# Kernel tuning notes

Hardware: AMD Instinct MI355X
Metric: run time of the kernel (lower is better)

## Reference

```python
import jax, jax.numpy as jnp
import numpy as np

VOCAB, D_MODEL, D_STATE, D_LATENT = 32000, 1024, 16, 32
SEQ, MAX_ITERS, TOL = 8192, 20, 1e-5


def _linear_params(k, out_d, in_d):
    lim = 1.0 / np.sqrt(in_d)  # eqx.nn.Linear default uniform init
    kw, kb = jax.random.split(k)
    W = jax.random.uniform(kw, (out_d, in_d), minval=-lim, maxval=lim, dtype=jnp.float32)
    b = jax.random.uniform(kb, (out_d,), minval=-lim, maxval=lim, dtype=jnp.float32)
    return W, b


def setup_inputs() -> dict:
    key = jax.random.key(0)
    ks = jax.random.split(key, 8)
    tokens = jax.random.randint(ks[0], (SEQ,), 0, VOCAB)
    emb = jax.random.normal(ks[1], (VOCAB, D_MODEL), dtype=jnp.float32) * 0.02
    Wf, bf = _linear_params(ks[2], D_LATENT // 2, D_STATE + D_MODEL)
    Wf2, bf2 = _linear_params(ks[3], D_LATENT // 2, D_STATE + D_MODEL)
    Wlam, blam = _linear_params(ks[4], D_STATE, D_LATENT + D_MODEL)
    Wu, bu = _linear_params(ks[5], D_STATE, D_LATENT + D_MODEL)
    Wout, bout = _linear_params(ks[6], D_MODEL, D_LATENT + D_STATE)
    return {"tokens": tokens, "emb": emb, "Wf": Wf, "bf": bf, "Wf2": Wf2, "bf2": bf2,
            "Wlam": Wlam, "blam": blam, "Wu": Wu, "bu": bu, "Wout": Wout, "bout": bout}


def reference(tokens, emb, Wf, bf, Wf2, bf2, Wlam, blam, Wu, bu, Wout, bout):
    x = emb[tokens]  # [S, d_model]

    def compute_lambda_u(z):
        zx = jnp.concatenate([z, x], axis=-1)              # [S, d_latent+d_model]
        lam = jax.nn.sigmoid(zx @ Wlam.T + blam)           # [S, d_state]
        u = zx @ Wu.T + bu                                 # [S, d_state]
        return lam, u

    def scan_h(lam, u):
        # h_t = lam_t * h_{t-1} + u_t via associative scan
        def binop(left, right):
            a1, b1 = left
            a2, b2 = right
            return (a1 * a2, a2 * b1 + b2)
        _, h = jax.lax.associative_scan(binop, (lam, u), axis=0)
        return h

    def f_theta(z, h_prev):
        hx = jnp.concatenate([h_prev, x], axis=-1)         # [S, d_state+d_model]
        alpha = jax.nn.sigmoid(hx @ Wf.T + bf)             # [S, d_latent//2]
        sigma = jax.nn.sigmoid(hx @ Wf2.T + bf2)
        u, v = jnp.split(z, 2, axis=-1)
        rho, beta, gamma = 30.0, 15.6, 0.26
        thresh = jnp.tanh(rho * (v - u))
        du = 1.0 - alpha * jnp.exp(beta * v) * (1.0 - gamma * (0.3 - u)) + sigma * thresh
        dv = -1.0 + alpha * jnp.exp(beta * u) * (1.0 + gamma * (0.3 - v)) + sigma * thresh
        return z + 0.001 * jnp.concatenate([du, dv], axis=-1)

    # Bounded fixed-point iteration with convergence freeze (emulates while_loop)
    def body(carry, _):
        z, z_prev, done = carry
        done = done | (jnp.linalg.norm(z - z_prev) < TOL)
        lam, u = compute_lambda_u(z)
        h = scan_h(lam, u)
        h_prev = jnp.concatenate([jnp.zeros((1, D_STATE), z.dtype), h[:-1]], axis=0)
        z_new = f_theta(z, h_prev)
        z_out = jnp.where(done, z, z_new)
        zp_out = jnp.where(done, z_prev, z)
        return (z_out, zp_out, done), None

    z0 = jnp.zeros((SEQ, D_LATENT), jnp.float32)
    zp0 = jnp.full((SEQ, D_LATENT), jnp.inf, jnp.float32)
    (z_star, _, _), _ = jax.lax.scan(body, (z0, zp0, jnp.array(False)), None, length=MAX_ITERS)

    lam, u = compute_lambda_u(z_star)
    h_star = scan_h(lam, u)
    zh = jnp.concatenate([z_star, h_star], axis=-1)        # [S, d_latent+d_state]
    return zh @ Wout.T + bout                              # [S, d_model]
```

## Files before the change

kernel.cpp:

```cpp
#include <hip/hip_runtime.h>

#define SEQ     8192
#define DM      1024
#define NB      256
#define CH      32
#define HALO    32
#define W       64
#define NT      512
#define MAXITERS 20

__device__ __forceinline__ float sigmoidf(float x) {
    return 1.0f / (1.0f + __expf(-x));
}
__device__ __forceinline__ float tanh_fast(float x) {
    const float e = __expf(2.0f * x);
    return 1.0f - 2.0f / (e + 1.0f);
}

__global__ __launch_bounds__(256) void k1_embed_proj(
    const int* __restrict__ tokens, const float* __restrict__ emb,
    const float* __restrict__ Wf,  const float* __restrict__ bf,
    const float* __restrict__ Wf2, const float* __restrict__ bf2,
    const float* __restrict__ Wlam,const float* __restrict__ blam,
    const float* __restrict__ Wu,  const float* __restrict__ bu,
    float* __restrict__ xlam, float* __restrict__ xu,
    float* __restrict__ xf,   float* __restrict__ xf2)
{
    __shared__ float4 xs4[8 * 256];
    const int tid = threadIdx.x;
    const int tokbase = blockIdx.x * 8;

    for (int j = tid; j < 8 * 256; j += 256) {
        const int tok = j >> 8, q = j & 255;
        const int row = tokens[tokbase + tok];
        const int qs = q ^ ((q >> 6) & 3);
        xs4[tok * 256 + qs] =
            *reinterpret_cast<const float4*>(emb + (size_t)row * DM + q * 4);
    }
    __syncthreads();

    const int r  = tid >> 2;
    const int kq = tid & 3;
    const int arr = r >> 4;
    const int c   = r & 15;

    const float* wb; const float* bv; float* dst; int wstr, woff;
    if (arr == 0)      { wb = Wlam; wstr = 1056; woff = 32; bv = blam; dst = xlam; }
    else if (arr == 1) { wb = Wu;   wstr = 1056; woff = 32; bv = bu;   dst = xu;   }
    else if (arr == 2) { wb = Wf;   wstr = 1040; woff = 16; bv = bf;   dst = xf;   }
    else               { wb = Wf2;  wstr = 1040; woff = 16; bv = bf2;  dst = xf2;  }

    const float4* wrow = reinterpret_cast<const float4*>(wb + (size_t)c * wstr + woff) + kq * 64;

    float acc[8];
    #pragma unroll
    for (int t = 0; t < 8; ++t) acc[t] = 0.0f;

    #pragma unroll 8
    for (int i = 0; i < 64; ++i) {
        const float4 w4 = wrow[i];
        const int gs = (kq * 64 + i) ^ kq;
        #pragma unroll
        for (int t = 0; t < 8; ++t) {
            const float4 x4 = xs4[t * 256 + gs];
            acc[t] += w4.x * x4.x + w4.y * x4.y + w4.z * x4.z + w4.w * x4.w;
        }
    }

    #pragma unroll
    for (int t = 0; t < 8; ++t) {
        acc[t] += __shfl_xor(acc[t], 1);
        acc[t] += __shfl_xor(acc[t], 2);
    }
    if (kq == 0) {
        const float bz = bv[c];
        #pragma unroll
        for (int t = 0; t < 8; ++t)
            dst[(size_t)(tokbase + t) * 16 + c] = acc[t] + bz;
    }
}

__global__ __launch_bounds__(NT, 2) void k2_fixed_point(
    const float* __restrict__ Wf,  const float* __restrict__ Wf2,
    const float* __restrict__ Wlam,const float* __restrict__ Wu,
    const float* __restrict__ xf,  const float* __restrict__ xf2,
    const float* __restrict__ xlam,const float* __restrict__ xu,
    const float* __restrict__ Wout,const float* __restrict__ bout,
    float* __restrict__ out)
{
    __shared__ float zsf[W * 32];
    __shared__ float hhT[16][W + 2];
    __shared__ float zhs[CH][48];

    const int tid = threadIdx.x;
    const int b = blockIdx.x;
    const int s0 = (b - 1) * CH;
    const int tq = tid & 31;
    const int c  = tid >> 5;

    for (int i = tid; i < W * 32; i += NT) zsf[i] = 0.0f;

    float2 wlu[32];
    #pragma unroll
    for (int s = 0; s < 32; ++s) {
        const int oj = (s & 1) ? 16 + (s >> 1) : (s >> 1);
        wlu[s].x = Wlam[(size_t)c * 1056 + oj];
        wlu[s].y = Wu  [(size_t)c * 1056 + oj];
    }
    float2 wfs[16];
    #pragma unroll
    for (int j = 0; j < 16; ++j) {
        wfs[j].x = Wf [(size_t)c * 1040 + j];
        wfs[j].y = Wf2[(size_t)c * 1040 + j];
    }

    float xl[2], xu_[2], xf_[2], x2_[2];
    bool act[2];
    #pragma unroll
    for (int k = 0; k < 2; ++k) {
        const int gt = s0 + tq + 32 * k;
        act[k] = (gt >= 0);
        const size_t gi = (size_t)(gt < 0 ? 0 : gt) * 16 + c;
        xl[k] = xlam[gi]; xu_[k] = xu[gi]; xf_[k] = xf[gi]; x2_[k] = xf2[gi];
    }
    __syncthreads();

    for (int r = 1; r <= MAXITERS + 1; ++r) {
        float ae[2], be[2];
        #pragma unroll
        for (int k = 0; k < 2; ++k) {
            const int tl = tq + 32 * k;
            const int sw = tl & 7;
            float2 acc = make_float2(xl[k], xu_[k]);
            #pragma unroll
            for (int g = 0; g < 8; ++g) {
                const float4 z4 = *reinterpret_cast<const float4*>(
                    &zsf[tl * 32 + ((g ^ sw) << 2)]);
                acc.x += z4.x * wlu[4*g+0].x;  acc.y += z4.x * wlu[4*g+0].y;
                acc.x += z4.y * wlu[4*g+1].x;  acc.y += z4.y * wlu[4*g+1].y;
                acc.x += z4.z * wlu[4*g+2].x;  acc.y += z4.z * wlu[4*g+2].y;
                acc.x += z4.w * wlu[4*g+3].x;  acc.y += z4.w * wlu[4*g+3].y;
            }
            ae[k] = act[k] ? sigmoidf(acc.x) : 0.0f;
            be[k] = act[k] ? acc.y : 0.0f;
        }

        float A = ae[0], B = be[0];
        #pragma unroll
        for (int d = 1; d < 32; d <<= 1) {
            float pA = __shfl_up(A, d, 32);
            float pB = __shfl_up(B, d, 32);
            pA = (tq >= d) ? pA : 1.0f;
            pB = (tq >= d) ? pB : 0.0f;
            B = A * pB + B;
            A = A * pA;
        }
        const float h0v = B;
        const float carry = __shfl(B, 31, 32);

        float A1 = ae[1], B1 = be[1];
        #pragma unroll
        for (int d = 1; d < 32; d <<= 1) {
            float pA = __shfl_up(A1, d, 32);
            float pB = __shfl_up(B1, d, 32);
            pA = (tq >= d) ? pA : 1.0f;
            pB = (tq >= d) ? pB : 0.0f;
            B1 = A1 * pB + B1;
            A1 = A1 * pA;
        }
        const float h1v = A1 * carry + B1;

        hhT[c][tq]      = h0v;
        hhT[c][tq + 32] = h1v;
        __syncthreads();

        if (r == MAXITERS + 1) {
            for (int i = tid; i < CH * 48; i += NT) {
                const int tt = i / 48, j = i - tt * 48;
                const int tl = HALO + tt;
                float v;
                if (j < 32) {
                    const int s = (j < 16) ? 2 * j : 2 * (j - 16) + 1;
                    v = zsf[tl * 32 + ((((s >> 2) ^ (tl & 7)) << 2) | (s & 3))];
                } else {
                    v = hhT[j - 32][tl];
                }
                zhs[tt][j] = v;
            }
            __syncthreads();
            #pragma unroll
            for (int q = 0; q < 2; ++q) {
                const int col = q * NT + tid;
                const float* wp = Wout + (size_t)col * 48;
                float4 wq[12];
                #pragma unroll
                for (int j = 0; j < 12; ++j)
                    wq[j] = *reinterpret_cast<const float4*>(wp + j * 4);
                const float bz = bout[col];
                for (int tt = 0; tt < CH; ++tt) {
                    float a = bz;
                    #pragma unroll
                    for (int j = 0; j < 12; ++j) {
                        const float4 z4 = *reinterpret_cast<const float4*>(&zhs[tt][j * 4]);
                        a += wq[j].x * z4.x + wq[j].y * z4.y
                           + wq[j].z * z4.z + wq[j].w * z4.w;
                    }
                    out[(size_t)(b * CH + tt) * 1024 + col] = a;
                }
            }
            break;
        }

        #pragma unroll
        for (int k = 0; k < 2; ++k) {
            const int tl = tq + 32 * k;
            const int tp = (tl == 0) ? 0 : tl - 1;
            float2 as2 = make_float2(xf_[k], x2_[k]);
            #pragma unroll
            for (int j = 0; j < 16; ++j) {
                const float hp = hhT[j][tp];
                as2.x += hp * wfs[j].x;
                as2.y += hp * wfs[j].y;
            }
            if (tl == 0) as2 = make_float2(xf_[k], x2_[k]);
            const float al_ = sigmoidf(as2.x);
            const float sg  = sigmoidf(as2.y);

            const int sw = tl & 7;
            const int pos = tl * 32 + ((((c >> 1) ^ sw) << 2) | ((2 * c) & 3));
            float2 uv = *reinterpret_cast<const float2*>(&zsf[pos]);
            const float th = tanh_fast(30.0f * (uv.y - uv.x));
            const float du = 0.001f * ( 1.0f - al_ * __expf(15.6f * uv.y) * (1.0f - 0.26f * (0.3f - uv.x)) + sg * th);
            const float dv = 0.001f * (-1.0f + al_ * __expf(15.6f * uv.x) * (1.0f + 0.26f * (0.3f - uv.y)) + sg * th);
            if (act[k]) {
                uv.x += du; uv.y += dv;
                *reinterpret_cast<float2*>(&zsf[pos]) = uv;
            }
        }
        __syncthreads();
    }
}

extern "C" void kernel_launch(void* const* d_in, const int* in_sizes, int n_in,
                              void* d_out, int out_size, void* d_ws, size_t ws_size,
                              hipStream_t stream) {
    (void)in_sizes; (void)n_in; (void)out_size; (void)ws_size;
    const int*   tokens = (const int*)  d_in[0];
    const float* emb    = (const float*)d_in[1];
    const float* Wf     = (const float*)d_in[2];
    const float* bf     = (const float*)d_in[3];
    const float* Wf2    = (const float*)d_in[4];
    const float* bf2    = (const float*)d_in[5];
    const float* Wlam   = (const float*)d_in[6];
    const float* blam   = (const float*)d_in[7];
    const float* Wu     = (const float*)d_in[8];
    const float* bu     = (const float*)d_in[9];
    const float* Wout   = (const float*)d_in[10];
    const float* bout   = (const float*)d_in[11];

    float* ws   = (float*)d_ws;
    float* xlam = ws;
    float* xu   = ws + 131072;
    float* xf   = ws + 262144;
    float* xf2  = ws + 393216;

    k1_embed_proj<<<SEQ / 8, 256, 0, stream>>>(tokens, emb, Wf, bf, Wf2, bf2,
                                               Wlam, blam, Wu, bu,
                                               xlam, xu, xf, xf2);

    k2_fixed_point<<<NB, NT, 0, stream>>>(Wf, Wf2, Wlam, Wu,
                                          xf, xf2, xlam, xu,
                                          Wout, bout, (float*)d_out);
}
```

Before: 119.2 us.

## Map one thread per token with full-wavefront scan in fixed-point kernel

```diff
diff --git a/kernel.cpp b/kernel.cpp
--- a/kernel.cpp
+++ b/kernel.cpp
@@ -6,7 +6,7 @@
 #define CH      32
 #define HALO    32
 #define W       64
-#define NT      512
+#define NT      1024
 #define MAXITERS 20
 
 __device__ __forceinline__ float sigmoidf(float x) {
@@ -52,9 +52,9 @@
 
     const float4* wrow = reinterpret_cast<const float4*>(wb + (size_t)c * wstr + woff) + kq * 64;
 
-    float acc[8];
-    #pragma unroll
-    for (int t = 0; t < 8; ++t) acc[t] = 0.0f;
+    float2 a2[8];
+    #pragma unroll
+    for (int t = 0; t < 8; ++t) a2[t] = make_float2(0.f, 0.f);
 
     #pragma unroll 8
     for (int i = 0; i < 64; ++i) {
@@ -63,24 +63,24 @@
         #pragma unroll
         for (int t = 0; t < 8; ++t) {
             const float4 x4 = xs4[t * 256 + gs];
-            acc[t] += w4.x * x4.x + w4.y * x4.y + w4.z * x4.z + w4.w * x4.w;
+            a2[t].x += w4.x * x4.x;  a2[t].y += w4.y * x4.y;
+            a2[t].x += w4.z * x4.z;  a2[t].y += w4.w * x4.w;
         }
     }
 
     #pragma unroll
     for (int t = 0; t < 8; ++t) {
-        acc[t] += __shfl_xor(acc[t], 1);
-        acc[t] += __shfl_xor(acc[t], 2);
-    }
-    if (kq == 0) {
-        const float bz = bv[c];
-        #pragma unroll
-        for (int t = 0; t < 8; ++t)
-            dst[(size_t)(tokbase + t) * 16 + c] = acc[t] + bz;
-    }
-}
-
-__global__ __launch_bounds__(NT, 2) void k2_fixed_point(
+        float acc = a2[t].x + a2[t].y;
+        acc += __shfl_xor(acc, 1);
+        acc += __shfl_xor(acc, 2);
+        if (kq == 0) {
+            const float bz = bv[c];
+            dst[(size_t)(tokbase + t) * 16 + c] = acc + bz;
+        }
+    }
+}
+
+__global__ __launch_bounds__(NT, 1) void k2_fixed_point(
     const float* __restrict__ Wf,  const float* __restrict__ Wf2,
     const float* __restrict__ Wlam,const float* __restrict__ Wu,
     const float* __restrict__ xf,  const float* __restrict__ xf2,
@@ -95,102 +95,78 @@
     const int tid = threadIdx.x;
     const int b = blockIdx.x;
     const int s0 = (b - 1) * CH;
-    const int tq = tid & 31;
-    const int c  = tid >> 5;
+    const int tl = tid & 63;
+    const int c  = __builtin_amdgcn_readfirstlane(tid >> 6);
 
     for (int i = tid; i < W * 32; i += NT) zsf[i] = 0.0f;
 
+    const float* WlamC = Wlam + (size_t)c * 1056;
+    const float* WuC   = Wu   + (size_t)c * 1056;
+    const float* WfC   = Wf   + (size_t)c * 1040;
+    const float* Wf2C  = Wf2  + (size_t)c * 1040;
     float2 wlu[32];
     #pragma unroll
     for (int s = 0; s < 32; ++s) {
         const int oj = (s & 1) ? 16 + (s >> 1) : (s >> 1);
-        wlu[s].x = Wlam[(size_t)c * 1056 + oj];
-        wlu[s].y = Wu  [(size_t)c * 1056 + oj];
+        wlu[s].x = WlamC[oj];
+        wlu[s].y = WuC[oj];
     }
     float2 wfs[16];
     #pragma unroll
     for (int j = 0; j < 16; ++j) {
-        wfs[j].x = Wf [(size_t)c * 1040 + j];
-        wfs[j].y = Wf2[(size_t)c * 1040 + j];
-    }
-
-    float xl[2], xu_[2], xf_[2], x2_[2];
-    bool act[2];
-    #pragma unroll
-    for (int k = 0; k < 2; ++k) {
-        const int gt = s0 + tq + 32 * k;
-        act[k] = (gt >= 0);
-        const size_t gi = (size_t)(gt < 0 ? 0 : gt) * 16 + c;
-        xl[k] = xlam[gi]; xu_[k] = xu[gi]; xf_[k] = xf[gi]; x2_[k] = xf2[gi];
-    }
+        wfs[j].x = WfC[j];
+        wfs[j].y = Wf2C[j];
+    }
+
+    const int gt = s0 + tl;
+    const bool act = (gt >= 0);
+    const size_t gi = (size_t)(act ? gt : 0) * 16 + c;
+    const float xl = xlam[gi], xuv = xu[gi], xfv = xf[gi], x2v = xf2[gi];
+    const int sw = tl & 7;
     __syncthreads();
 
     for (int r = 1; r <= MAXITERS + 1; ++r) {
-        float ae[2], be[2];
+        float2 acc = make_float2(xl, xuv);
         #pragma unroll
-        for (int k = 0; k < 2; ++k) {
-            const int tl = tq + 32 * k;
-            const int sw = tl & 7;
-            float2 acc = make_float2(xl[k], xu_[k]);
-            #pragma unroll
-            for (int g = 0; g < 8; ++g) {
-                const float4 z4 = *reinterpret_cast<const float4*>(
-                    &zsf[tl * 32 + ((g ^ sw) << 2)]);
-                acc.x += z4.x * wlu[4*g+0].x;  acc.y += z4.x * wlu[4*g+0].y;
-                acc.x += z4.y * wlu[4*g+1].x;  acc.y += z4.y * wlu[4*g+1].y;
-                acc.x += z4.z * wlu[4*g+2].x;  acc.y += z4.z * wlu[4*g+2].y;
-                acc.x += z4.w * wlu[4*g+3].x;  acc.y += z4.w * wlu[4*g+3].y;
-            }
-            ae[k] = act[k] ? sigmoidf(acc.x) : 0.0f;
-            be[k] = act[k] ? acc.y : 0.0f;
-        }
-
-        float A = ae[0], B = be[0];
+        for (int g = 0; g < 8; ++g) {
+            const float4 z4 = *reinterpret_cast<const float4*>(
+                &zsf[tl * 32 + ((g ^ sw) << 2)]);
+            acc.x += z4.x * wlu[4*g+0].x;  acc.y += z4.x * wlu[4*g+0].y;
+            acc.x += z4.y * wlu[4*g+1].x;  acc.y += z4.y * wlu[4*g+1].y;
+            acc.x += z4.z * wlu[4*g+2].x;  acc.y += z4.z * wlu[4*g+2].y;
+            acc.x += z4.w * wlu[4*g+3].x;  acc.y += z4.w * wlu[4*g+3].y;
+        }
+        float A = act ? sigmoidf(acc.x) : 0.0f;
+        float B = act ? acc.y : 0.0f;
+
         #pragma unroll
-        for (int d = 1; d < 32; d <<= 1) {
-            float pA = __shfl_up(A, d, 32);
-            float pB = __shfl_up(B, d, 32);
-            pA = (tq >= d) ? pA : 1.0f;
-            pB = (tq >= d) ? pB : 0.0f;
+        for (int d = 1; d < 64; d <<= 1) {
+            float pA = __shfl_up(A, d, 64);
+            float pB = __shfl_up(B, d, 64);
+            pA = (tl >= d) ? pA : 1.0f;
+            pB = (tl >= d) ? pB : 0.0f;
             B = A * pB + B;
             A = A * pA;
         }
-        const float h0v = B;
-        const float carry = __shfl(B, 31, 32);
-
-        float A1 = ae[1], B1 = be[1];
-        #pragma unroll
-        for (int d = 1; d < 32; d <<= 1) {
-            float pA = __shfl_up(A1, d, 32);
-            float pB = __shfl_up(B1, d, 32);
-            pA = (tq >= d) ? pA : 1.0f;
-            pB = (tq >= d) ? pB : 0.0f;
-            B1 = A1 * pB + B1;
-            A1 = A1 * pA;
-        }
-        const float h1v = A1 * carry + B1;
-
-        hhT[c][tq]      = h0v;
-        hhT[c][tq + 32] = h1v;
+        hhT[c][tl] = B;
         __syncthreads();
 
         if (r == MAXITERS + 1) {
             for (int i = tid; i < CH * 48; i += NT) {
                 const int tt = i / 48, j = i - tt * 48;
-                const int tl = HALO + tt;
+                const int tle = HALO + tt;
                 float v;
                 if (j < 32) {
                     const int s = (j < 16) ? 2 * j : 2 * (j - 16) + 1;
-                    v = zsf[tl * 32 + ((((s >> 2) ^ (tl & 7)) << 2) | (s & 3))];
+                    v = zsf[tle * 32 + ((((s >> 2) ^ (tle & 7)) << 2) | (s & 3))];
                 } else {
-                    v = hhT[j - 32][tl];
+                    v = hhT[j - 32][tle];
                 }
                 zhs[tt][j] = v;
             }
             __syncthreads();
-            #pragma unroll
-            for (int q = 0; q < 2; ++q) {
-                const int col = q * NT + tid;
+            {
+                const int col = tid;
                 const float* wp = Wout + (size_t)col * 48;
                 float4 wq[12];
                 #pragma unroll
@@ -211,28 +187,25 @@
             break;
         }
 
-        #pragma unroll
-        for (int k = 0; k < 2; ++k) {
-            const int tl = tq + 32 * k;
+        {
             const int tp = (tl == 0) ? 0 : tl - 1;
-            float2 as2 = make_float2(xf_[k], x2_[k]);
+            float2 as2 = make_float2(xfv, x2v);
             #pragma unroll
             for (int j = 0; j < 16; ++j) {
                 const float hp = hhT[j][tp];
                 as2.x += hp * wfs[j].x;
                 as2.y += hp * wfs[j].y;
             }
-            if (tl == 0) as2 = make_float2(xf_[k], x2_[k]);
+            if (tl == 0) as2 = make_float2(xfv, x2v);
             const float al_ = sigmoidf(as2.x);
             const float sg  = sigmoidf(as2.y);
 
-            const int sw = tl & 7;
             const int pos = tl * 32 + ((((c >> 1) ^ sw) << 2) | ((2 * c) & 3));
             float2 uv = *reinterpret_cast<const float2*>(&zsf[pos]);
             const float th = tanh_fast(30.0f * (uv.y - uv.x));
             const float du = 0.001f * ( 1.0f - al_ * __expf(15.6f * uv.y) * (1.0f - 0.26f * (0.3f - uv.x)) + sg * th);
             const float dv = 0.001f * (-1.0f + al_ * __expf(15.6f * uv.x) * (1.0f + 0.26f * (0.3f - uv.y)) + sg * th);
-            if (act[k]) {
+            if (act) {
                 uv.x += du; uv.y += dv;
                 *reinterpret_cast<float2*>(&zsf[pos]) = uv;
             }
```

New measurement: 122.6 us. 1.03x slower.

## Retile embed projection to 4 rows x 2 tokens per thread with float2 accumulators

Applied to the files above, without the earlier changes.

```diff
diff --git a/kernel.cpp b/kernel.cpp
--- a/kernel.cpp
+++ b/kernel.cpp
@@ -33,16 +33,17 @@
     for (int j = tid; j < 8 * 256; j += 256) {
         const int tok = j >> 8, q = j & 255;
         const int row = tokens[tokbase + tok];
-        const int qs = q ^ ((q >> 6) & 3);
+        const int qs = q ^ ((tok & 3) << 1) ^ ((q >> 6) & 3);
         xs4[tok * 256 + qs] =
             *reinterpret_cast<const float4*>(emb + (size_t)row * DM + q * 4);
     }
     __syncthreads();
 
-    const int r  = tid >> 2;
-    const int kq = tid & 3;
-    const int arr = r >> 4;
-    const int c   = r & 15;
+    const int kq    = tid & 3;
+    const int tpair = (tid >> 2) & 3;
+    const int rgrp  = tid >> 4;
+    const int arr   = rgrp >> 2;
+    const int c0    = (rgrp & 3) * 4;
 
     const float* wb; const float* bv; float* dst; int wstr, woff;
     if (arr == 0)      { wb = Wlam; wstr = 1056; woff = 32; bv = blam; dst = xlam; }
@@ -50,34 +51,50 @@
     else if (arr == 2) { wb = Wf;   wstr = 1040; woff = 16; bv = bf;   dst = xf;   }
     else               { wb = Wf2;  wstr = 1040; woff = 16; bv = bf2;  dst = xf2;  }
 
-    const float4* wrow = reinterpret_cast<const float4*>(wb + (size_t)c * wstr + woff) + kq * 64;
-
-    float acc[8];
-    #pragma unroll
-    for (int t = 0; t < 8; ++t) acc[t] = 0.0f;
-
-    #pragma unroll 8
+    const float4* wr[4];
+    #pragma unroll
+    for (int rr = 0; rr < 4; ++rr)
+        wr[rr] = reinterpret_cast<const float4*>(wb + (size_t)(c0 + rr) * wstr + woff) + kq * 64;
+
+    float2 a2[4][2];
+    #pragma unroll
+    for (int rr = 0; rr < 4; ++rr)
+        #pragma unroll
+        for (int tt = 0; tt < 2; ++tt) a2[rr][tt] = make_float2(0.f, 0.f);
+
+    const int t0 = tpair * 2;
+    #pragma unroll 4
     for (int i = 0; i < 64; ++i) {
-        const float4 w4 = wrow[i];
-        const int gs = (kq * 64 + i) ^ kq;
-        #pragma unroll
-        for (int t = 0; t < 8; ++t) {
-            const float4 x4 = xs4[t * 256 + gs];
-            acc[t] += w4.x * x4.x + w4.y * x4.y + w4.z * x4.z + w4.w * x4.w;
-        }
-    }
-
-    #pragma unroll
-    for (int t = 0; t < 8; ++t) {
-        acc[t] += __shfl_xor(acc[t], 1);
-        acc[t] += __shfl_xor(acc[t], 2);
-    }
-    if (kq == 0) {
-        const float bz = bv[c];
-        #pragma unroll
-        for (int t = 0; t < 8; ++t)
-            dst[(size_t)(tokbase + t) * 16 + c] = acc[t] + bz;
-    }
+        const int q = kq * 64 + i;
+        float4 w4[4];
+        #pragma unroll
+        for (int rr = 0; rr < 4; ++rr) w4[rr] = wr[rr][i];
+        float4 x4[2];
+        #pragma unroll
+        for (int tt = 0; tt < 2; ++tt) {
+            const int tok = t0 + tt;
+            const int gs = q ^ ((tok & 3) << 1) ^ ((q >> 6) & 3);
+            x4[tt] = xs4[tok * 256 + gs];
+        }
+        #pragma unroll
+        for (int rr = 0; rr < 4; ++rr)
+            #pragma unroll
+            for (int tt = 0; tt < 2; ++tt) {
+                a2[rr][tt].x += w4[rr].x * x4[tt].x + w4[rr].z * x4[tt].z;
+                a2[rr][tt].y += w4[rr].y * x4[tt].y + w4[rr].w * x4[tt].w;
+            }
+    }
+
+    #pragma unroll
+    for (int rr = 0; rr < 4; ++rr)
+        #pragma unroll
+        for (int tt = 0; tt < 2; ++tt) {
+            float acc = a2[rr][tt].x + a2[rr][tt].y;
+            acc += __shfl_xor(acc, 1);
+            acc += __shfl_xor(acc, 2);
+            if (kq == 0)
+                dst[(size_t)(tokbase + t0 + tt) * 16 + (c0 + rr)] = acc + bv[c0 + rr];
+        }
 }
 
 __global__ __launch_bounds__(NT, 2) void k2_fixed_point(
```

Result: slower. 201.3 us (+68.8%).
